# Performance work log

Measured on AMD Instinct MI355X. Metric: run time of the kernel, lower is better.

Reference implementation:

```python
import jax, jax.numpy as jnp
import numpy as np

ALPHA = 1e-4
MARGIN = 100.0
K = 3
DROP_P = 0.7


def setup_inputs() -> dict:
    key = jax.random.key(0)
    ks = jax.random.split(key, 8)
    NC, B, T, F = 10, 32, 200, 2048
    return {
        "abnr_feat_magn": jax.random.uniform(ks[0], (B, T), jnp.float32),
        "norm_feat_magn": jax.random.uniform(ks[1], (B, T), jnp.float32),
        "abnr_feats": jax.random.normal(ks[2], (NC, B, T, F), jnp.float32),
        "norm_feats": jax.random.normal(ks[3], (NC, B, T, F), jnp.float32),
        "abnr_sls": jax.random.uniform(ks[4], (B, T), jnp.float32),
        "norm_sls": jax.random.uniform(ks[5], (B, T), jnp.float32),
        "abnr_drop_u": jax.random.uniform(ks[6], (B, T), jnp.float32),
        "norm_drop_u": jax.random.uniform(ks[7], (B, T), jnp.float32),
    }


def _topk_idx(magn, drop_u):
    # Dropout(0.7) on ones_like, multiplied into the magnitudes before top-k.
    mask = (drop_u >= DROP_P).astype(magn.dtype) / (1.0 - DROP_P)
    _, idx = jax.lax.top_k(magn * mask, K)  # (B, K)
    return idx


def _gather_mean_norm(feats, idx):
    # feats: (NC, B, T, F); idx: (B, K) -> gather over T per crop, mean over K, L2 over F.
    sel = jnp.take_along_axis(feats, idx[None, :, :, None], axis=2)  # (NC, B, K, F)
    mean_feat = sel.mean(axis=2)  # (NC, B, F)  == torch.cat over crops -> (NC*B, F)
    return jnp.linalg.norm(mean_feat, axis=-1).reshape(-1)  # (NC*B,)


def _clamped_log(x):
    # torch BCELoss clamps log terms at -100
    return jnp.clip(jnp.log(x), -100.0, None)


def reference(abnr_feat_magn, norm_feat_magn, abnr_feats, norm_feats,
              abnr_sls, norm_sls, abnr_drop_u, norm_drop_u):
    idx_abnr = _topk_idx(abnr_feat_magn, abnr_drop_u)  # (B, K)
    idx_norm = _topk_idx(norm_feat_magn, norm_drop_u)

    l2_abn = _gather_mean_norm(abnr_feats, idx_abnr)   # (NC*B,)
    l2_nor = _gather_mean_norm(norm_feats, idx_norm)
    loss_abn = jnp.abs(MARGIN - l2_abn)
    loss_rtfm = jnp.mean((loss_abn + l2_nor) ** 2)

    vls_abn = jnp.take_along_axis(abnr_sls, idx_abnr, axis=1).mean(axis=1)  # (B,)
    vls_nor = jnp.take_along_axis(norm_sls, idx_norm, axis=1).mean(axis=1)
    loss_bcea = -jnp.mean(_clamped_log(vls_abn))          # BCE vs target 1
    loss_bcen = -jnp.mean(_clamped_log(1.0 - vls_nor))    # BCE vs target 0
    loss_vls = loss_bcea + loss_bcen

    return ALPHA * loss_rtfm, loss_vls
```

## Files before the change

### kernel.cpp

```cpp
#include <hip/hip_runtime.h>
#include <math.h>

#define BB 32
#define TT 200
#define NCC 10
#define FF 2048
#define KK 3
#define NBLK (2 * NCC * BB * 4)

__device__ inline void wave_argmax(float& v, int& i) {
    #pragma unroll
    for (int m = 1; m < 64; m <<= 1) {
        float ov = __shfl_xor(v, m);
        int   oi = __shfl_xor(i, m);
        if (ov > v || (ov == v && oi < i)) { v = ov; i = oi; }
    }
}

__device__ inline float wave_sum(float v) {
    #pragma unroll
    for (int m = 1; m < 64; m <<= 1) v += __shfl_xor(v, m);
    return v;
}

__global__ __launch_bounds__(64) void fused_kernel(
        const float* __restrict__ abnr_magn,
        const float* __restrict__ norm_magn,
        const float* __restrict__ abnr_feats,
        const float* __restrict__ norm_feats,
        const float* __restrict__ abnr_sls,
        const float* __restrict__ norm_sls,
        const float* __restrict__ abnr_u,
        const float* __restrict__ norm_u,
        float* __restrict__ partial ,
        float* __restrict__ bce     ) {
    const int blk  = blockIdx.x;
    const int fc   = blk & 3;
    const int r    = blk >> 2;
    const int b    = r % BB;
    const int sn   = r / BB;
    const int side = sn / NCC;
    const int nc   = sn % NCC;
    const int lane = threadIdx.x;

    const float* feats = side ? norm_feats : abnr_feats;
    const float* magn  = side ? norm_magn  : abnr_magn;
    const float* u     = side ? norm_u     : abnr_u;

    const float scale = 1.0f / (1.0f - 0.7f);
    float vv[4];
    int   tv[4];
    if (lane < TT / 4) {
        float4 mg = *(const float4*)(magn + b * TT + lane * 4);
        float4 uu = *(const float4*)(u    + b * TT + lane * 4);
        vv[0] = mg.x * ((uu.x >= 0.7f) ? scale : 0.0f);
        vv[1] = mg.y * ((uu.y >= 0.7f) ? scale : 0.0f);
        vv[2] = mg.z * ((uu.z >= 0.7f) ? scale : 0.0f);
        vv[3] = mg.w * ((uu.w >= 0.7f) ? scale : 0.0f);
        #pragma unroll
        for (int j = 0; j < 4; ++j) tv[j] = lane * 4 + j;
    } else {
        #pragma unroll
        for (int j = 0; j < 4; ++j) { vv[j] = -INFINITY; tv[j] = 1 << 30; }
    }
    int id[KK];
    #pragma unroll
    for (int k = 0; k < KK; ++k) {
        float bv = -INFINITY;
        int   bi = 1 << 30;
        #pragma unroll
        for (int j = 0; j < 4; ++j)
            if (vv[j] > bv || (vv[j] == bv && tv[j] < bi)) { bv = vv[j]; bi = tv[j]; }
        wave_argmax(bv, bi);
        id[k] = bi;
        #pragma unroll
        for (int j = 0; j < 4; ++j)
            if (tv[j] == bi) vv[j] = -INFINITY;
    }

    const size_t base = (size_t)(nc * BB + b) * (TT * FF) + (size_t)fc * (FF / 4) + lane * 4;
    const float* p0 = feats + base + (size_t)id[0] * FF;
    const float* p1 = feats + base + (size_t)id[1] * FF;
    const float* p2 = feats + base + (size_t)id[2] * FF;
    float4 a0 = *(const float4*)(p0);
    float4 a1 = *(const float4*)(p1);
    float4 a2 = *(const float4*)(p2);
    float4 b0 = *(const float4*)(p0 + 256);
    float4 b1 = *(const float4*)(p1 + 256);
    float4 b2 = *(const float4*)(p2 + 256);

    float m, acc = 0.0f;
    m = a0.x + a1.x + a2.x; acc += m * m;
    m = a0.y + a1.y + a2.y; acc += m * m;
    m = a0.z + a1.z + a2.z; acc += m * m;
    m = a0.w + a1.w + a2.w; acc += m * m;
    m = b0.x + b1.x + b2.x; acc += m * m;
    m = b0.y + b1.y + b2.y; acc += m * m;
    m = b0.z + b1.z + b2.z; acc += m * m;
    m = b0.w + b1.w + b2.w; acc += m * m;

    acc = wave_sum(acc);
    if (lane == 0) partial[blk] = acc;

    if (nc == 0 && fc == 0 && lane == 0) {
        const float* sls = side ? norm_sls : abnr_sls;
        float v = (sls[b * TT + id[0]] + sls[b * TT + id[1]] +
                   sls[b * TT + id[2]]) * (1.0f / 3.0f);
        bce[side * BB + b] = side ? fmaxf(logf(1.0f - v), -100.0f)
                                  : fmaxf(logf(v), -100.0f);
    }
}

__global__ __launch_bounds__(64) void final_kernel(
        const float* __restrict__ partial, const float* __restrict__ bce,
        float* __restrict__ out) {
    const int lane = threadIdx.x;
    const float third = 1.0f / 3.0f;

    float s = 0.0f;
    #pragma unroll
    for (int it = 0; it < (NCC * BB) / 64; ++it) {
        int i = it * 64 + lane;
        float4 pa4 = *(const float4*)(partial + 4 * i);
        float4 pn4 = *(const float4*)(partial + 4 * (NCC * BB + i));
        float pa = (pa4.x + pa4.y) + (pa4.z + pa4.w);
        float pn = (pn4.x + pn4.y) + (pn4.z + pn4.w);
        float l2a = sqrtf(pa) * third;
        float l2n = sqrtf(pn) * third;
        float t = fabsf(100.0f - l2a) + l2n;
        s += t * t;
    }
    s = wave_sum(s);

    float s2 = bce[lane];
    s2 = wave_sum(s2);

    if (lane == 0) {
        out[0] = 1e-4f * (s * (1.0f / (float)(NCC * BB)));
        out[1] = -s2 * (1.0f / (float)BB);
    }
}

extern "C" void kernel_launch(void* const* d_in, const int* in_sizes, int n_in,
                              void* d_out, int out_size, void* d_ws, size_t ws_size,
                              hipStream_t stream) {
    const float* abnr_magn  = (const float*)d_in[0];
    const float* norm_magn  = (const float*)d_in[1];
    const float* abnr_feats = (const float*)d_in[2];
    const float* norm_feats = (const float*)d_in[3];
    const float* abnr_sls   = (const float*)d_in[4];
    const float* norm_sls   = (const float*)d_in[5];
    const float* abnr_u     = (const float*)d_in[6];
    const float* norm_u     = (const float*)d_in[7];
    float* out = (float*)d_out;

    float* bce     = (float*)d_ws;
    float* partial = (float*)((char*)d_ws + 4096);

    fused_kernel<<<NBLK, 64, 0, stream>>>(abnr_magn, norm_magn,
                                          abnr_feats, norm_feats,
                                          abnr_sls, norm_sls,
                                          abnr_u, norm_u,
                                          partial, bce);
    final_kernel<<<1, 64, 0, stream>>>(partial, bce, out);
}
```

Baseline: 12.03 us.

## Merge gather and final reduction into one kernel with flag-based completion

Replaces the two-kernel launch with a single kernel. Block 0 spins on per-block sentinel flags, then performs the final loss reduction. Worker blocks now use 256 threads covering half a feature row each, with the top-k computed by one wave and shared through LDS. This removes the second kernel launch and its dependency gap, at the cost of a spinning block, flag traffic, and an extra intra-block barrier and reduction.

```diff
diff --git a/kernel.cpp b/kernel.cpp
--- a/kernel.cpp
+++ b/kernel.cpp
@@ -6,7 +6,9 @@
 #define NCC 10
 #define FF 2048
 #define KK 3
-#define NBLK (2 * NCC * BB * 4)
+#define NWRITE (2 * NCC * BB * 2)
+
+#define SENT(w) (0x9E3779B9u * (unsigned)((w) + 1))
 
 __device__ inline void wave_argmax(float& v, int& i) {
     #pragma unroll
@@ -23,7 +25,7 @@
     return v;
 }
 
-__global__ __launch_bounds__(64) void fused_kernel(
+__global__ __launch_bounds__(256) void mono_kernel(
         const float* __restrict__ abnr_magn,
         const float* __restrict__ norm_magn,
         const float* __restrict__ abnr_feats,
@@ -32,112 +34,129 @@
         const float* __restrict__ norm_sls,
         const float* __restrict__ abnr_u,
         const float* __restrict__ norm_u,
-        float* __restrict__ partial ,
-        float* __restrict__ bce     ) {
-    const int blk  = blockIdx.x;
-    const int fc   = blk & 3;
-    const int r    = blk >> 2;
+        float*    __restrict__ partial ,
+        float*    __restrict__ bce     ,
+        unsigned* __restrict__ flags   ,
+        float*    __restrict__ out) {
+    const int bid = blockIdx.x;
+    const int tid = threadIdx.x;
+    const int lane = tid & 63;
+    const int wav  = tid >> 6;
+
+    if (bid == 0) {
+        #pragma unroll
+        for (int k = 0; k < NWRITE / 256; ++k) {
+            const int w = tid + k * 256;
+            const unsigned sent = SENT(w);
+            while (__hip_atomic_load(&flags[w], __ATOMIC_ACQUIRE,
+                                     __HIP_MEMORY_SCOPE_AGENT) != sent)
+                __builtin_amdgcn_s_sleep(2);
+            flags[w] = 0u;
+        }
+        __syncthreads();
+
+        if (wav == 0) {
+            const float third = 1.0f / 3.0f;
+            float s = 0.0f;
+            #pragma unroll
+            for (int k = 0; k < (NCC * BB) / 64; ++k) {
+                int i = lane + 64 * k;
+                float2 pa2 = *(const float2*)(partial + 2 * i);
+                float2 pn2 = *(const float2*)(partial + 2 * (NCC * BB + i));
+                float l2a = sqrtf(pa2.x + pa2.y) * third;
+                float l2n = sqrtf(pn2.x + pn2.y) * third;
+                float t = fabsf(100.0f - l2a) + l2n;
+                s += t * t;
+            }
+            s = wave_sum(s);
+
+            float s2 = bce[lane];
+            s2 = wave_sum(s2);
+
+            if (lane == 0) {
+                out[0] = 1e-4f * (s * (1.0f / (float)(NCC * BB)));
+                out[1] = -s2 * (1.0f / (float)BB);
+            }
+        }
+        return;
+    }
+
+    const int w    = bid - 1;
+    const int fc   = w & 1;
+    const int r    = w >> 1;
     const int b    = r % BB;
     const int sn   = r / BB;
     const int side = sn / NCC;
     const int nc   = sn % NCC;
-    const int lane = threadIdx.x;
 
     const float* feats = side ? norm_feats : abnr_feats;
-    const float* magn  = side ? norm_magn  : abnr_magn;
-    const float* u     = side ? norm_u     : abnr_u;
 
-    const float scale = 1.0f / (1.0f - 0.7f);
-    float vv[4];
-    int   tv[4];
-    if (lane < TT / 4) {
-        float4 mg = *(const float4*)(magn + b * TT + lane * 4);
-        float4 uu = *(const float4*)(u    + b * TT + lane * 4);
-        vv[0] = mg.x * ((uu.x >= 0.7f) ? scale : 0.0f);
-        vv[1] = mg.y * ((uu.y >= 0.7f) ? scale : 0.0f);
-        vv[2] = mg.z * ((uu.z >= 0.7f) ? scale : 0.0f);
-        vv[3] = mg.w * ((uu.w >= 0.7f) ? scale : 0.0f);
+    __shared__ int   s_idx[KK];
+    __shared__ float s_red[4];
+
+    if (wav == 0) {
+        const float* magn = side ? norm_magn : abnr_magn;
+        const float* u    = side ? norm_u    : abnr_u;
+        const float scale = 1.0f / (1.0f - 0.7f);
+        float vv[4];
+        int   tv[4];
+        if (lane < TT / 4) {
+            float4 mg = *(const float4*)(magn + b * TT + lane * 4);
+            float4 uu = *(const float4*)(u    + b * TT + lane * 4);
+            vv[0] = mg.x * ((uu.x >= 0.7f) ? scale : 0.0f);
+            vv[1] = mg.y * ((uu.y >= 0.7f) ? scale : 0.0f);
+            vv[2] = mg.z * ((uu.z >= 0.7f) ? scale : 0.0f);
+            vv[3] = mg.w * ((uu.w >= 0.7f) ? scale : 0.0f);
+            #pragma unroll
+            for (int j = 0; j < 4; ++j) tv[j] = lane * 4 + j;
+        } else {
+            #pragma unroll
+            for (int j = 0; j < 4; ++j) { vv[j] = -INFINITY; tv[j] = 1 << 30; }
+        }
+        int id[KK];
         #pragma unroll
-        for (int j = 0; j < 4; ++j) tv[j] = lane * 4 + j;
-    } else {
-        #pragma unroll
-        for (int j = 0; j < 4; ++j) { vv[j] = -INFINITY; tv[j] = 1 << 30; }
+        for (int k = 0; k < KK; ++k) {
+            float bv = -INFINITY;
+            int   bi = 1 << 30;
+            #pragma unroll
+            for (int j = 0; j < 4; ++j)
+                if (vv[j] > bv || (vv[j] == bv && tv[j] < bi)) { bv = vv[j]; bi = tv[j]; }
+            wave_argmax(bv, bi);
+            id[k] = bi;
+            #pragma unroll
+            for (int j = 0; j < 4; ++j)
+                if (tv[j] == bi) vv[j] = -INFINITY;
+        }
+        if (lane < KK) s_idx[lane] = id[lane];
+
+        if (nc == 0 && fc == 0 && lane == 0) {
+            const float* sls = side ? norm_sls : abnr_sls;
+            float v = (sls[b * TT + id[0]] + sls[b * TT + id[1]] +
+                       sls[b * TT + id[2]]) * (1.0f / 3.0f);
+            bce[side * BB + b] = side ? fmaxf(logf(1.0f - v), -100.0f)
+                                      : fmaxf(logf(v), -100.0f);
+        }
     }
-    int id[KK];
-    #pragma unroll
-    for (int k = 0; k < KK; ++k) {
-        float bv = -INFINITY;
-        int   bi = 1 << 30;
-        #pragma unroll
-        for (int j = 0; j < 4; ++j)
-            if (vv[j] > bv || (vv[j] == bv && tv[j] < bi)) { bv = vv[j]; bi = tv[j]; }
-        wave_argmax(bv, bi);
-        id[k] = bi;
-        #pragma unroll
-        for (int j = 0; j < 4; ++j)
-            if (tv[j] == bi) vv[j] = -INFINITY;
-    }
+    __syncthreads();
+    const int id0 = s_idx[0], id1 = s_idx[1], id2 = s_idx[2];
 
-    const size_t base = (size_t)(nc * BB + b) * (TT * FF) + (size_t)fc * (FF / 4) + lane * 4;
-    const float* p0 = feats + base + (size_t)id[0] * FF;
-    const float* p1 = feats + base + (size_t)id[1] * FF;
-    const float* p2 = feats + base + (size_t)id[2] * FF;
-    float4 a0 = *(const float4*)(p0);
-    float4 a1 = *(const float4*)(p1);
-    float4 a2 = *(const float4*)(p2);
-    float4 b0 = *(const float4*)(p0 + 256);
-    float4 b1 = *(const float4*)(p1 + 256);
-    float4 b2 = *(const float4*)(p2 + 256);
-
+    const size_t base = (size_t)(nc * BB + b) * (TT * FF) + (size_t)fc * (FF / 2) + tid * 4;
+    float4 x0 = *(const float4*)(feats + base + (size_t)id0 * FF);
+    float4 x1 = *(const float4*)(feats + base + (size_t)id1 * FF);
+    float4 x2 = *(const float4*)(feats + base + (size_t)id2 * FF);
     float m, acc = 0.0f;
-    m = a0.x + a1.x + a2.x; acc += m * m;
-    m = a0.y + a1.y + a2.y; acc += m * m;
-    m = a0.z + a1.z + a2.z; acc += m * m;
-    m = a0.w + a1.w + a2.w; acc += m * m;
-    m = b0.x + b1.x + b2.x; acc += m * m;
-    m = b0.y + b1.y + b2.y; acc += m * m;
-    m = b0.z + b1.z + b2.z; acc += m * m;
-    m = b0.w + b1.w + b2.w; acc += m * m;
+    m = x0.x + x1.x + x2.x; acc += m * m;
+    m = x0.y + x1.y + x2.y; acc += m * m;
+    m = x0.z + x1.z + x2.z; acc += m * m;
+    m = x0.w + x1.w + x2.w; acc += m * m;
 
     acc = wave_sum(acc);
-    if (lane == 0) partial[blk] = acc;
-
-    if (nc == 0 && fc == 0 && lane == 0) {
-        const float* sls = side ? norm_sls : abnr_sls;
-        float v = (sls[b * TT + id[0]] + sls[b * TT + id[1]] +
-                   sls[b * TT + id[2]]) * (1.0f / 3.0f);
-        bce[side * BB + b] = side ? fmaxf(logf(1.0f - v), -100.0f)
-                                  : fmaxf(logf(v), -100.0f);
-    }
-}
-
-__global__ __launch_bounds__(64) void final_kernel(
-        const float* __restrict__ partial, const float* __restrict__ bce,
-        float* __restrict__ out) {
-    const int lane = threadIdx.x;
-    const float third = 1.0f / 3.0f;
-
-    float s = 0.0f;
-    #pragma unroll
-    for (int it = 0; it < (NCC * BB) / 64; ++it) {
-        int i = it * 64 + lane;
-        float4 pa4 = *(const float4*)(partial + 4 * i);
-        float4 pn4 = *(const float4*)(partial + 4 * (NCC * BB + i));
-        float pa = (pa4.x + pa4.y) + (pa4.z + pa4.w);
-        float pn = (pn4.x + pn4.y) + (pn4.z + pn4.w);
-        float l2a = sqrtf(pa) * third;
-        float l2n = sqrtf(pn) * third;
-        float t = fabsf(100.0f - l2a) + l2n;
-        s += t * t;
-    }
-    s = wave_sum(s);
-
-    float s2 = bce[lane];
-    s2 = wave_sum(s2);
-
-    if (lane == 0) {
-        out[0] = 1e-4f * (s * (1.0f / (float)(NCC * BB)));
-        out[1] = -s2 * (1.0f / (float)BB);
+    if (lane == 0) s_red[wav] = acc;
+    __syncthreads();
+    if (tid == 0) {
+        partial[w] = s_red[0] + s_red[1] + s_red[2] + s_red[3];
+        __hip_atomic_store(&flags[w], SENT(w), __ATOMIC_RELEASE,
+                           __HIP_MEMORY_SCOPE_AGENT);
     }
 }
 
@@ -154,13 +173,13 @@
     const float* norm_u     = (const float*)d_in[7];
     float* out = (float*)d_out;
 
-    float* bce     = (float*)d_ws;
-    float* partial = (float*)((char*)d_ws + 4096);
+    float*    bce     = (float*)d_ws;
+    float*    partial = (float*)((char*)d_ws + 4096);
+    unsigned* flags   = (unsigned*)((char*)d_ws + 32768);
 
-    fused_kernel<<<NBLK, 64, 0, stream>>>(abnr_magn, norm_magn,
-                                          abnr_feats, norm_feats,
-                                          abnr_sls, norm_sls,
-                                          abnr_u, norm_u,
-                                          partial, bce);
-    final_kernel<<<1, 64, 0, stream>>>(partial, bce, out);
+    mono_kernel<<<NWRITE + 1, 256, 0, stream>>>(abnr_magn, norm_magn,
+                                                abnr_feats, norm_feats,
+                                                abnr_sls, norm_sls,
+                                                abnr_u, norm_u,
+                                                partial, bce, flags, out);
 }
```

New measurement: 24.99 us. 2.08x slower.
